# Kernel optimization log

Hardware: AMD Instinct MI355X
Metric: run time of the kernel (lower is better)

Reference implementation:

```python
import jax, jax.numpy as jnp
import numpy as np

CH = 512


def _maxpool2(t):
    # 2x2 max pool, stride 2, NCHW
    B, C, H, W = t.shape
    return t.reshape(B, C, H // 2, 2, W // 2, 2).max(axis=(3, 5))


def setup_inputs() -> dict:
    key = jax.random.key(0)
    ks = jax.random.split(key, 6)
    B, C, H, W = 8, CH, 64, 64
    x = jax.random.normal(ks[0], (B, C, H, W), dtype=jnp.float32)
    # 1x1 conv weights stored as [out_ch, in_ch]
    w_theta = jax.random.normal(ks[1], (C // 8, C), dtype=jnp.float32) * (1.0 / np.sqrt(C))
    w_phi = jax.random.normal(ks[2], (C // 8, C), dtype=jnp.float32) * (1.0 / np.sqrt(C))
    w_g = jax.random.normal(ks[3], (C // 2, C), dtype=jnp.float32) * (1.0 / np.sqrt(C))
    w_o = jax.random.normal(ks[4], (C, C // 2), dtype=jnp.float32) * (1.0 / np.sqrt(C // 2))
    # gamma is a learned scalar (init 0.0 in the original); use 0.5 so the
    # attention branch contributes to the output for testing purposes.
    gamma = jnp.float32(0.5)
    return {"x": x, "w_theta": w_theta, "w_phi": w_phi, "w_g": w_g, "w_o": w_o, "gamma": gamma}


def reference(x, w_theta, w_phi, w_g, w_o, gamma):
    B, C, H, W = x.shape
    c8, c2 = C // 8, C // 2
    # 1x1 conv projections
    theta = jnp.einsum('bchw,oc->bohw', x, w_theta)           # [B, C/8, H, W]
    phi = _maxpool2(jnp.einsum('bchw,oc->bohw', x, w_phi))    # [B, C/8, H/2, W/2]
    g = _maxpool2(jnp.einsum('bchw,oc->bohw', x, w_g))        # [B, C/2, H/2, W/2]
    n, m = H * W, (H * W) // 4
    theta = theta.reshape(B, c8, n)
    phi = phi.reshape(B, c8, m)
    g = g.reshape(B, c2, m)
    # unscaled attention scores: [B, n, m]
    beta = jax.nn.softmax(jnp.einsum('bcn,bcm->bnm', theta, phi), axis=-1)
    # attend: g @ beta^T -> [B, C/2, n]
    att = jnp.einsum('bcm,bnm->bcn', g, beta).reshape(B, c2, H, W)
    o = jnp.einsum('bchw,oc->bohw', att, w_o)                 # [B, C, H, W]
    return gamma * o + x
```

## Files before the change

kernel.cpp:

```cpp
#include <hip/hip_runtime.h>
#include <math.h>

constexpr int CB = 8;
constexpr int CC = 512;
constexpr int CN = 4096;
constexpr int CM = 1024;
constexpr int C8 = 64;
constexpr int C2 = 256;

typedef __attribute__((ext_vector_type(8))) short short8;
typedef __attribute__((ext_vector_type(8))) _Float16 half8;
typedef __attribute__((ext_vector_type(4))) float f32x4;

__device__ inline unsigned short f2bf(float f) {
  unsigned int u = __float_as_uint(f);
  return (unsigned short)((u + 0x7FFFu + ((u >> 16) & 1u)) >> 16);
}
__device__ inline unsigned short f16bits(float f) {
  union { _Float16 h; unsigned short u; } c;
  c.h = (_Float16)f;
  return c.u;
}

__global__ __launch_bounds__(256)
void conv_w(const float* __restrict__ wt, const float* __restrict__ wp,
            const float* __restrict__ wg, const float* __restrict__ wo,
            _Float16* __restrict__ wth, _Float16* __restrict__ wtl,
            _Float16* __restrict__ wph, _Float16* __restrict__ wpl,
            _Float16* __restrict__ wgf, unsigned short* __restrict__ woh) {
  const int i = blockIdx.x * 256 + threadIdx.x;
  if (i < 32768) {
    float a = wt[i];
    _Float16 h = (_Float16)a;
    wth[i] = h; wtl[i] = (_Float16)(a - (float)h);
    a = wp[i];
    h = (_Float16)a;
    wph[i] = h; wpl[i] = (_Float16)(a - (float)h);
  }
  wgf[i] = (_Float16)wg[i];
  woh[i] = f2bf(wo[i]);
}

__global__ __launch_bounds__(256)
void xpose(const float* __restrict__ X, _Float16* __restrict__ xT) {
  __shared__ __align__(16) float raw[64][68];
  const int b = blockIdx.z, c0 = blockIdx.y * 64, n0 = blockIdx.x * 64;
  const float* Xb = X + ((size_t)b * CC + c0) * CN + n0;
  const int tid = threadIdx.x;
#pragma unroll
  for (int it = 0; it < 4; ++it) {
    const int idx = it * 256 + tid;
    const int row = idx >> 4, col4 = (idx & 15) * 4;
    *(float4*)&raw[row][col4] = *(const float4*)&Xb[(size_t)row * CN + col4];
  }
  __syncthreads();
  unsigned short* Yb = (unsigned short*)(xT + ((size_t)b * CN + n0) * CC + c0);
#pragma unroll
  for (int it = 0; it < 4; ++it) {
    const int idx = it * 256 + tid;
    const int n = idx >> 4, c4 = (idx & 15) * 4;
    ushort4 o;
    o.x = f16bits(raw[c4 + 0][n]);
    o.y = f16bits(raw[c4 + 1][n]);
    o.z = f16bits(raw[c4 + 2][n]);
    o.w = f16bits(raw[c4 + 3][n]);
    *(ushort4*)&Yb[(size_t)n * CC + c4] = o;
  }
}

__global__ __launch_bounds__(256)
void proj_th(const _Float16* __restrict__ Wh, const _Float16* __restrict__ Wl,
             const _Float16* __restrict__ xT, _Float16* __restrict__ thT) {
  __shared__ __align__(16) unsigned short LT[64][68];
  const int b = blockIdx.y, n0 = blockIdx.x * 64;
  const int tid = threadIdx.x;
  const int w = tid >> 6, l = tid & 63;
  const int l15 = l & 15, quad = l >> 4;
  f32x4 acc[4] = {};
  const _Float16* Brow = xT + (size_t)(b * CN + n0 + w * 16 + l15) * CC;
  for (int k0 = 0; k0 < CC; k0 += 32) {
    const half8 bfr = *(const half8*)&Brow[k0 + quad * 8];
#pragma unroll
    for (int i = 0; i < 4; ++i) {
      const half8 ah = *(const half8*)&Wh[(size_t)(i * 16 + l15) * CC + k0 + quad * 8];
      const half8 al = *(const half8*)&Wl[(size_t)(i * 16 + l15) * CC + k0 + quad * 8];
      acc[i] = __builtin_amdgcn_mfma_f32_16x16x32_f16(ah, bfr, acc[i], 0, 0, 0);
      acc[i] = __builtin_amdgcn_mfma_f32_16x16x32_f16(al, bfr, acc[i], 0, 0, 0);
    }
  }
#pragma unroll
  for (int i = 0; i < 4; ++i)
#pragma unroll
    for (int r = 0; r < 4; ++r)
      LT[w * 16 + l15][i * 16 + quad * 4 + r] = f16bits(acc[i][r]);
  __syncthreads();
  unsigned short* Yb = (unsigned short*)(thT + (size_t)(b * CN + n0) * C8);
#pragma unroll
  for (int it = 0; it < 4; ++it) {
    const int idx = it * 256 + tid;
    const int pos = idx >> 4, c4 = (idx & 15) * 4;
    ushort4 v = *(const ushort4*)&LT[pos][c4];
    *(ushort4*)&Yb[(size_t)pos * C8 + c4] = v;
  }
}

__global__ __launch_bounds__(256)
void proj_pg(const _Float16* __restrict__ Wph, const _Float16* __restrict__ Wpl,
             const _Float16* __restrict__ Wg, const _Float16* __restrict__ xT,
             _Float16* __restrict__ phT, unsigned short* __restrict__ gbf) {
  __shared__ float Pbuf[2][64][33];
  const int b = blockIdx.z, mt = blockIdx.y, tile = blockIdx.x;
  const int n0 = tile * 256;
  const int tid = threadIdx.x;
  const int w = tid >> 6, l = tid & 63;
  const int l15 = l & 15, quad = l >> 4;
  const bool isphi = (mt == 0);
  const _Float16* Ah = isphi ? Wph : (Wg + (size_t)(mt - 1) * 64 * CC);
  f32x4 acc[4][4] = {};
  const _Float16* Bbase = xT + (size_t)(b * CN + n0 + w * 64) * CC;
  for (int k0 = 0; k0 < CC; k0 += 32) {
    half8 bf[4], ah[4];
#pragma unroll
    for (int j = 0; j < 4; ++j)
      bf[j] = *(const half8*)&Bbase[(size_t)(j * 16 + l15) * CC + k0 + quad * 8];
#pragma unroll
    for (int i = 0; i < 4; ++i)
      ah[i] = *(const half8*)&Ah[(size_t)(i * 16 + l15) * CC + k0 + quad * 8];
#pragma unroll
    for (int i = 0; i < 4; ++i)
#pragma unroll
      for (int j = 0; j < 4; ++j)
        acc[i][j] = __builtin_amdgcn_mfma_f32_16x16x32_f16(ah[i], bf[j], acc[i][j], 0, 0, 0);
    if (isphi) {
      half8 al[4];
#pragma unroll
      for (int i = 0; i < 4; ++i)
        al[i] = *(const half8*)&Wpl[(size_t)(i * 16 + l15) * CC + k0 + quad * 8];
#pragma unroll
      for (int i = 0; i < 4; ++i)
#pragma unroll
        for (int j = 0; j < 4; ++j)
          acc[i][j] = __builtin_amdgcn_mfma_f32_16x16x32_f16(al[i], bf[j], acc[i][j], 0, 0, 0);
    }
  }
  const bool owner = ((l15 & 1) == 0);
  const int colh = l15 >> 1;
  if (w & 1) {
#pragma unroll
    for (int i = 0; i < 4; ++i)
#pragma unroll
      for (int j = 0; j < 4; ++j)
#pragma unroll
        for (int r = 0; r < 4; ++r) {
          float v = acc[i][j][r];
          float o = __shfl_xor(v, 1);
          v = fmaxf(v, o);
          if (owner) Pbuf[w >> 1][i * 16 + quad * 4 + r][j * 8 + colh] = v;
        }
  }
  __syncthreads();
  if (!(w & 1)) {
    const int pr = tile * 2 + (w >> 1);
    unsigned short* phB = (unsigned short*)(phT + ((size_t)b * CM + pr * 32) * C8);
#pragma unroll
    for (int i = 0; i < 4; ++i)
#pragma unroll
      for (int j = 0; j < 4; ++j)
#pragma unroll
        for (int r = 0; r < 4; ++r) {
          float v = acc[i][j][r];
          float o = __shfl_xor(v, 1);
          v = fmaxf(v, o);
          if (owner) {
            const int oc = i * 16 + quad * 4 + r;
            const int col = j * 8 + colh;
            v = fmaxf(v, Pbuf[w >> 1][oc][col]);
            if (isphi)
              phB[(size_t)col * C8 + oc] = f16bits(v);
            else
              gbf[((size_t)b * C2 + (mt - 1) * 64 + oc) * CM + pr * 32 + col] = f2bf(v);
          }
        }
  }
}

__global__ __launch_bounds__(256)
void attn_v3(const _Float16* __restrict__ thT, const _Float16* __restrict__ phT,
             const unsigned short* __restrict__ gbf,
             unsigned short* __restrict__ attbf) {
  __shared__ __align__(16) unsigned short Pl[4][4][16][40];
  const int b = blockIdx.y;
  const int q0 = blockIdx.x * 64;
  const int tid = threadIdx.x;
  const int w = tid >> 6, l = tid & 63;
  const int l15 = l & 15, quad = l >> 4;
  half8 tb[4][2];
#pragma unroll
  for (int qs = 0; qs < 4; ++qs)
#pragma unroll
    for (int kc = 0; kc < 2; ++kc)
      tb[qs][kc] = *(const half8*)&thT[(size_t)(b * CN + q0 + qs * 16 + l15) * C8 +
                                       kc * 32 + quad * 8];
  f32x4 acc[4][4] = {};
  float dnp[4] = {0.f, 0.f, 0.f, 0.f};
  const _Float16* phB = phT + (size_t)b * CM * C8;
  const unsigned short* gB = gbf + (size_t)b * C2 * CM;

  for (int j0 = 0; j0 < CM; j0 += 32) {
    half8 pa[2][2];
#pragma unroll
    for (int jt = 0; jt < 2; ++jt)
#pragma unroll
      for (int kc = 0; kc < 2; ++kc)
        pa[jt][kc] = *(const half8*)&phB[(size_t)(j0 + jt * 16 + l15) * C8 +
                                         kc * 32 + quad * 8];
#pragma unroll
    for (int qs = 0; qs < 4; ++qs) {
      f32x4 S0 = {0.f, 0.f, 0.f, 0.f}, S1 = {0.f, 0.f, 0.f, 0.f};
      S0 = __builtin_amdgcn_mfma_f32_16x16x32_f16(pa[0][0], tb[qs][0], S0, 0, 0, 0);
      S0 = __builtin_amdgcn_mfma_f32_16x16x32_f16(pa[0][1], tb[qs][1], S0, 0, 0, 0);
      S1 = __builtin_amdgcn_mfma_f32_16x16x32_f16(pa[1][0], tb[qs][0], S1, 0, 0, 0);
      S1 = __builtin_amdgcn_mfma_f32_16x16x32_f16(pa[1][1], tb[qs][1], S1, 0, 0, 0);
      float e0[4], e1[4];
#pragma unroll
      for (int r = 0; r < 4; ++r) { e0[r] = __expf(S0[r]); e1[r] = __expf(S1[r]); }
      dnp[qs] += (e0[0] + e0[1]) + (e0[2] + e0[3]) +
                 (e1[0] + e1[1]) + (e1[2] + e1[3]);
      ushort4 w0, w1;
      w0.x = f2bf(e0[0]); w0.y = f2bf(e0[1]); w0.z = f2bf(e0[2]); w0.w = f2bf(e0[3]);
      w1.x = f2bf(e1[0]); w1.y = f2bf(e1[1]); w1.z = f2bf(e1[2]); w1.w = f2bf(e1[3]);
      *(ushort4*)&Pl[w][qs][l15][quad * 4] = w0;
      *(ushort4*)&Pl[w][qs][l15][16 + quad * 4] = w1;
    }
    short8 pfrag[4];
#pragma unroll
    for (int qs = 0; qs < 4; ++qs)
      pfrag[qs] = *(const short8*)&Pl[w][qs][l15][quad * 8];
#pragma unroll
    for (int ct = 0; ct < 4; ++ct) {
      const short8 gf = *(const short8*)&gB[(size_t)(w * 64 + ct * 16 + l15) * CM +
                                            j0 + quad * 8];
#pragma unroll
      for (int qs = 0; qs < 4; ++qs)
        acc[qs][ct] = __builtin_amdgcn_mfma_f32_16x16x32_bf16(pfrag[qs], gf,
                                                              acc[qs][ct], 0, 0, 0);
    }
  }
  unsigned short* attB = attbf + (size_t)(b * CN + q0) * C2;
#pragma unroll
  for (int qs = 0; qs < 4; ++qs) {
    float d = dnp[qs];
    d += __shfl_xor(d, 16);
    d += __shfl_xor(d, 32);
    const float inv = 1.0f / d;
#pragma unroll
    for (int r = 0; r < 4; ++r) {
      const float iv = __shfl(inv, quad * 4 + r);
      const int row = qs * 16 + quad * 4 + r;
#pragma unroll
      for (int ct = 0; ct < 4; ++ct)
        attB[(size_t)row * C2 + w * 64 + ct * 16 + l15] =
            f2bf(acc[qs][ct][r] * iv);
    }
  }
}

__global__ __launch_bounds__(256)
void oproj_mfma(const unsigned short* __restrict__ woh,
                const unsigned short* __restrict__ attbf,
                const float* __restrict__ X, const float* __restrict__ gamma,
                float* __restrict__ out) {
  const int b = blockIdx.z;
  const int mt = blockIdx.y;
  const int n0 = blockIdx.x * 256;
  const int tid = threadIdx.x;
  const int w = tid >> 6, l = tid & 63;
  const int l15 = l & 15, quad = l >> 4;
  const unsigned short* Bb = attbf + (size_t)b * CN * C2;
  f32x4 acc[4][4] = {};
  for (int k0 = 0; k0 < C2; k0 += 32) {
    short8 a[4], bb[4];
#pragma unroll
    for (int i = 0; i < 4; ++i)
      a[i] = *(const short8*)&woh[(size_t)(mt * 64 + i * 16 + l15) * C2 + k0 + quad * 8];
#pragma unroll
    for (int j = 0; j < 4; ++j)
      bb[j] = *(const short8*)&Bb[(size_t)(n0 + w * 64 + j * 16 + l15) * C2 + k0 + quad * 8];
#pragma unroll
    for (int i = 0; i < 4; ++i)
#pragma unroll
      for (int j = 0; j < 4; ++j)
        acc[i][j] = __builtin_amdgcn_mfma_f32_16x16x32_bf16(a[i], bb[j], acc[i][j], 0, 0, 0);
  }
  const float gm = gamma[0];
#pragma unroll
  for (int i = 0; i < 4; ++i)
#pragma unroll
    for (int j = 0; j < 4; ++j)
#pragma unroll
      for (int r = 0; r < 4; ++r) {
        const int c = mt * 64 + i * 16 + quad * 4 + r;
        const int pos = n0 + w * 64 + j * 16 + l15;
        const size_t idx = ((size_t)b * CC + c) * CN + pos;
        out[idx] = X[idx] + gm * acc[i][j][r];
      }
}

extern "C" void kernel_launch(void* const* d_in, const int* in_sizes, int n_in,
                              void* d_out, int out_size, void* d_ws, size_t ws_size,
                              hipStream_t stream) {
  const float* x       = (const float*)d_in[0];
  const float* w_theta = (const float*)d_in[1];
  const float* w_phi   = (const float*)d_in[2];
  const float* w_g     = (const float*)d_in[3];
  const float* w_o     = (const float*)d_in[4];
  const float* gamma   = (const float*)d_in[5];
  float* out = (float*)d_out;
  char* wsb = (char*)d_ws;

  _Float16*       xT    = (_Float16*)(wsb + 0);
  _Float16*       thT   = (_Float16*)(wsb + 33554432);
  _Float16*       phT   = (_Float16*)(wsb + 37748736);
  unsigned short* gbf   = (unsigned short*)(wsb + 38797312);
  _Float16*       wth   = (_Float16*)(wsb + 42991616);
  _Float16*       wtl   = (_Float16*)(wsb + 43057152);
  _Float16*       wph   = (_Float16*)(wsb + 43122688);
  _Float16*       wpl   = (_Float16*)(wsb + 43188224);
  _Float16*       wgf   = (_Float16*)(wsb + 43253760);
  unsigned short* woh   = (unsigned short*)(wsb + 43515904);
  unsigned short* attbf = (unsigned short*)(wsb + 0);

  dim3 blk(256);
  conv_w<<<512, blk, 0, stream>>>(w_theta, w_phi, w_g, w_o,
                                  wth, wtl, wph, wpl, wgf, woh);
  xpose<<<dim3(64, 8, CB), blk, 0, stream>>>(x, xT);
  proj_th<<<dim3(64, CB), blk, 0, stream>>>(wth, wtl, xT, thT);
  proj_pg<<<dim3(16, 5, CB), blk, 0, stream>>>(wph, wpl, wgf, xT, phT, gbf);
  attn_v3<<<dim3(64, CB), blk, 0, stream>>>(thT, phT, gbf, attbf);
  oproj_mfma<<<dim3(16, 8, CB), blk, 0, stream>>>(woh, attbf, x, gamma, out);
}
```

Baseline: 343.6 us.

## Halve attention query tile, pack bf16 cheaply, stage oproj epilogue via LDS

The attention kernel now handles 32 queries per block instead of 64, doubling the grid to 1024 blocks so more CUs stay busy, at the cost of reloading phi and g twice as often. The float-to-bf16 conversion for softmax probabilities uses a round-half-up add plus a byte permute that packs two values per instruction, replacing per-element round-to-nearest-even. The output projection epilogue stages accumulators through shared memory so the X read and output write become coalesced float4 rows, adding barriers.

```diff
diff --git a/kernel.cpp b/kernel.cpp
--- a/kernel.cpp
+++ b/kernel.cpp
@@ -20,6 +20,10 @@
   union { _Float16 h; unsigned short u; } c;
   c.h = (_Float16)f;
   return c.u;
+}
+__device__ inline unsigned int pk_bf(float e0, float e1) {
+  return __builtin_amdgcn_perm(__float_as_uint(e1) + 0x8000u,
+                               __float_as_uint(e0) + 0x8000u, 0x07060302u);
 }
 
 __global__ __launch_bounds__(256)
@@ -185,24 +189,24 @@
 }
 
 __global__ __launch_bounds__(256)
-void attn_v3(const _Float16* __restrict__ thT, const _Float16* __restrict__ phT,
+void attn_v4(const _Float16* __restrict__ thT, const _Float16* __restrict__ phT,
              const unsigned short* __restrict__ gbf,
              unsigned short* __restrict__ attbf) {
-  __shared__ __align__(16) unsigned short Pl[4][4][16][40];
+  __shared__ __align__(16) unsigned short Pl[4][2][16][40];
   const int b = blockIdx.y;
-  const int q0 = blockIdx.x * 64;
+  const int q0 = blockIdx.x * 32;
   const int tid = threadIdx.x;
   const int w = tid >> 6, l = tid & 63;
   const int l15 = l & 15, quad = l >> 4;
-  half8 tb[4][2];
-#pragma unroll
-  for (int qs = 0; qs < 4; ++qs)
+  half8 tb[2][2];
+#pragma unroll
+  for (int qs = 0; qs < 2; ++qs)
 #pragma unroll
     for (int kc = 0; kc < 2; ++kc)
       tb[qs][kc] = *(const half8*)&thT[(size_t)(b * CN + q0 + qs * 16 + l15) * C8 +
                                        kc * 32 + quad * 8];
-  f32x4 acc[4][4] = {};
-  float dnp[4] = {0.f, 0.f, 0.f, 0.f};
+  f32x4 acc[2][4] = {};
+  float dnp[2] = {0.f, 0.f};
   const _Float16* phB = phT + (size_t)b * CM * C8;
   const unsigned short* gB = gbf + (size_t)b * C2 * CM;
 
@@ -215,7 +219,7 @@
         pa[jt][kc] = *(const half8*)&phB[(size_t)(j0 + jt * 16 + l15) * C8 +
                                          kc * 32 + quad * 8];
 #pragma unroll
-    for (int qs = 0; qs < 4; ++qs) {
+    for (int qs = 0; qs < 2; ++qs) {
       f32x4 S0 = {0.f, 0.f, 0.f, 0.f}, S1 = {0.f, 0.f, 0.f, 0.f};
       S0 = __builtin_amdgcn_mfma_f32_16x16x32_f16(pa[0][0], tb[qs][0], S0, 0, 0, 0);
       S0 = __builtin_amdgcn_mfma_f32_16x16x32_f16(pa[0][1], tb[qs][1], S0, 0, 0, 0);
@@ -226,29 +230,29 @@
       for (int r = 0; r < 4; ++r) { e0[r] = __expf(S0[r]); e1[r] = __expf(S1[r]); }
       dnp[qs] += (e0[0] + e0[1]) + (e0[2] + e0[3]) +
                  (e1[0] + e1[1]) + (e1[2] + e1[3]);
-      ushort4 w0, w1;
-      w0.x = f2bf(e0[0]); w0.y = f2bf(e0[1]); w0.z = f2bf(e0[2]); w0.w = f2bf(e0[3]);
-      w1.x = f2bf(e1[0]); w1.y = f2bf(e1[1]); w1.z = f2bf(e1[2]); w1.w = f2bf(e1[3]);
-      *(ushort4*)&Pl[w][qs][l15][quad * 4] = w0;
-      *(ushort4*)&Pl[w][qs][l15][16 + quad * 4] = w1;
-    }
-    short8 pfrag[4];
-#pragma unroll
-    for (int qs = 0; qs < 4; ++qs)
+      uint2 v0, v1;
+      v0.x = pk_bf(e0[0], e0[1]); v0.y = pk_bf(e0[2], e0[3]);
+      v1.x = pk_bf(e1[0], e1[1]); v1.y = pk_bf(e1[2], e1[3]);
+      *(uint2*)&Pl[w][qs][l15][quad * 4] = v0;
+      *(uint2*)&Pl[w][qs][l15][16 + quad * 4] = v1;
+    }
+    short8 pfrag[2];
+#pragma unroll
+    for (int qs = 0; qs < 2; ++qs)
       pfrag[qs] = *(const short8*)&Pl[w][qs][l15][quad * 8];
 #pragma unroll
     for (int ct = 0; ct < 4; ++ct) {
       const short8 gf = *(const short8*)&gB[(size_t)(w * 64 + ct * 16 + l15) * CM +
                                             j0 + quad * 8];
 #pragma unroll
-      for (int qs = 0; qs < 4; ++qs)
+      for (int qs = 0; qs < 2; ++qs)
         acc[qs][ct] = __builtin_amdgcn_mfma_f32_16x16x32_bf16(pfrag[qs], gf,
                                                               acc[qs][ct], 0, 0, 0);
     }
   }
   unsigned short* attB = attbf + (size_t)(b * CN + q0) * C2;
 #pragma unroll
-  for (int qs = 0; qs < 4; ++qs) {
+  for (int qs = 0; qs < 2; ++qs) {
     float d = dnp[qs];
     d += __shfl_xor(d, 16);
     d += __shfl_xor(d, 32);
@@ -270,6 +274,7 @@
                 const unsigned short* __restrict__ attbf,
                 const float* __restrict__ X, const float* __restrict__ gamma,
                 float* __restrict__ out) {
+  __shared__ __align__(16) float Ls[16][260];
   const int b = blockIdx.z;
   const int mt = blockIdx.y;
   const int n0 = blockIdx.x * 256;
@@ -293,17 +298,29 @@
         acc[i][j] = __builtin_amdgcn_mfma_f32_16x16x32_bf16(a[i], bb[j], acc[i][j], 0, 0, 0);
   }
   const float gm = gamma[0];
-#pragma unroll
-  for (int i = 0; i < 4; ++i)
+  const int tr = tid >> 4;
+  const int cl = (tid & 15) * 4;
+  for (int i = 0; i < 4; ++i) {
+    __syncthreads();
 #pragma unroll
     for (int j = 0; j < 4; ++j)
 #pragma unroll
-      for (int r = 0; r < 4; ++r) {
-        const int c = mt * 64 + i * 16 + quad * 4 + r;
-        const int pos = n0 + w * 64 + j * 16 + l15;
-        const size_t idx = ((size_t)b * CC + c) * CN + pos;
-        out[idx] = X[idx] + gm * acc[i][j][r];
-      }
+      for (int r = 0; r < 4; ++r)
+        Ls[quad * 4 + r][w * 64 + j * 16 + l15] = acc[i][j][r];
+    __syncthreads();
+    const size_t row = (size_t)b * CC + mt * 64 + i * 16 + tr;
+    const float* Xr = X + row * CN + n0;
+    float* Or = out + row * CN + n0;
+#pragma unroll
+    for (int k = 0; k < 4; ++k) {
+      const int col = k * 64 + cl;
+      const float4 xv = *(const float4*)&Xr[col];
+      const float4 lv = *(const float4*)&Ls[tr][col];
+      float4 o = {xv.x + gm * lv.x, xv.y + gm * lv.y,
+                  xv.z + gm * lv.z, xv.w + gm * lv.w};
+      *(float4*)&Or[col] = o;
+    }
+  }
 }
 
 extern "C" void kernel_launch(void* const* d_in, const int* in_sizes, int n_in,
@@ -336,6 +353,6 @@
   xpose<<<dim3(64, 8, CB), blk, 0, stream>>>(x, xT);
   proj_th<<<dim3(64, CB), blk, 0, stream>>>(wth, wtl, xT, thT);
   proj_pg<<<dim3(16, 5, CB), blk, 0, stream>>>(wph, wpl, wgf, xT, phT, gbf);
-  attn_v3<<<dim3(64, CB), blk, 0, stream>>>(thT, phT, gbf, attbf);
+  attn_v4<<<dim3(128, CB), blk, 0, stream>>>(thT, phT, gbf, attbf);
   oproj_mfma<<<dim3(16, 8, CB), blk, 0, stream>>>(woh, attbf, x, gamma, out);
 }
```

New measurement: 378.9 us. 10.3% more time.
